# Optimization experiments

Measured on AMD Instinct MI355X. Metric: run time of the kernel, lower is better.

Reference implementation:

```python
import jax, jax.numpy as jnp
import numpy as np

B, C, T = 16, 128, 4096
Q, K = 8, 1024


def setup_inputs() -> dict:
    key = jax.random.key(0)
    k1, k2 = jax.random.split(key)
    latents = jax.random.normal(k1, (B, C, T), dtype=jnp.float32)
    embeddings = jax.random.normal(k2, (Q, K, C), dtype=jnp.float32)
    return {"latents": latents, "embeddings": embeddings}


def reference(latents, embeddings):
    # latents: [B, C, T]; embeddings: [Q, K, C]
    b, c, t = latents.shape
    q = embeddings.shape[0]
    flat = latents.transpose(0, 2, 1).reshape(-1, c)  # [N, C], N = B*T

    def stage(carry, emb):
        residual, qsum, closs = carry
        # squared euclidean distances [N, K] via expansion identity
        d = ((residual * residual).sum(axis=1, keepdims=True)
             - 2.0 * residual @ emb.T
             + (emb * emb).sum(axis=1))
        idx = jnp.argmin(d, axis=1)          # [N]
        quant = emb[idx]                     # [N, C] gather
        closs = closs + jnp.mean((residual - jax.lax.stop_gradient(quant)) ** 2)
        return (residual - quant, qsum + quant, closs), idx

    init = (flat, jnp.zeros_like(flat), jnp.zeros((), dtype=flat.dtype))
    (_, qsum, closs), codes = jax.lax.scan(stage, init, embeddings)

    quantized = qsum.reshape(b, t, c).transpose(0, 2, 1)       # [B, C, T]
    codes = codes.reshape(q, b, t).transpose(1, 0, 2)          # [B, Q, T]
    commitment_loss = closs / q
    codebook_loss = jnp.zeros((), dtype=latents.dtype)
    return quantized, codes, commitment_loss, codebook_loss
```

## Files before the change

### kernel.cpp

```cpp
#include <hip/hip_runtime.h>

#define Bq 16
#define Cc 128
#define Tt 4096
#define Qq 8
#define Kk 1024
#define Nn (Bq*Tt)

#define ROWS 128
#define NTC  256
#define KCH  32
#define NTILES (Kk/NTC)
#define KCHUNKS (Cc/KCH)
#define NCHUNK (NTILES*KCHUNKS)

typedef float f32x4 __attribute__((ext_vector_type(4)));
typedef float f32x8 __attribute__((ext_vector_type(8)));
typedef int   i32x8 __attribute__((ext_vector_type(8)));

static __device__ __forceinline__ f32x8 splat8(float x) {
    f32x8 v = {x, x, x, x, x, x, x, x};
    return v;
}

__global__ __launch_bounds__(256) void ee_kernel(const float* __restrict__ emb,
                                                 float* __restrict__ ee,
                                                 double* __restrict__ closs) {
    int i = blockIdx.x * 256 + threadIdx.x;
    if (i == 0) *closs = 0.0;
    if (i < Qq * Kk) {
        const float* e = emb + (size_t)i * Cc;
        float s0 = 0.f, s1 = 0.f, s2 = 0.f, s3 = 0.f;
#pragma unroll
        for (int c = 0; c < Cc; c += 4) {
            s0 = fmaf(e[c],     e[c],     s0);
            s1 = fmaf(e[c + 1], e[c + 1], s1);
            s2 = fmaf(e[c + 2], e[c + 2], s2);
            s3 = fmaf(e[c + 3], e[c + 3], s3);
        }
        ee[i] = (s0 + s1) + (s2 + s3);
    }
}

__global__ __launch_bounds__(512, 2) void vq_kernel(
    const float* __restrict__ latents,
    const float* __restrict__ emb,
    const float* __restrict__ ee,
    float* __restrict__ quantized,
    float* __restrict__ codes,
    double* __restrict__ closs)
{
    extern __shared__ float smem[];
    float* r_lds  = smem;
    float* B_lds  = smem + Cc * ROWS;
    float* rrp    = B_lds + 2 * KCH * NTC;
    float* rr_lds = rrp + 4 * ROWS;
    int*   win    = (int*)(rr_lds + ROWS);

    const int t   = threadIdx.x;
    const int tx  = t & 31;
    const int ty  = t >> 5;
    const int un  = t & 127;
    const int ukg = t >> 7;
    const int cl  = t >> 1;
    const int hk  = (t & 1) * 16;

    const int rowbase = blockIdx.x * ROWS;
    const int bb  = rowbase >> 12;
    const int tt0 = rowbase & (Tt - 1);

    {
        const float* lb = latents + (size_t)bb * Cc * Tt + tt0 + un;
        float part = 0.f;
#pragma unroll
        for (int j = 0; j < KCH; ++j) {
            int k = ukg * KCH + j;
            float v = lb[(size_t)k * Tt];
            r_lds[k * ROWS + un] = v;
            part = fmaf(v, v, part);
        }
        rrp[ukg * ROWS + un] = part;
    }
    __syncthreads();
    if (t < ROWS)
        rr_lds[t] = (rrp[t] + rrp[ROWS + t]) + (rrp[2 * ROWS + t] + rrp[3 * ROWS + t]);
    __syncthreads();

    for (int q = 0; q < Qq; ++q) {
        const float* eq = emb + (size_t)q * Kk * Cc;

        f32x8 best_ = splat8(3.4e38f);
        i32x8 bk_   = {0, 0, 0, 0, 0, 0, 0, 0};
        f32x8 rr8   = *(const f32x8*)&rr_lds[ty * 8];

        {
            const float* src = eq + (size_t)cl * Cc + hk;
            f32x4 pf0 = *(const f32x4*)(src);
            f32x4 pf1 = *(const f32x4*)(src + 4);
            f32x4 pf2 = *(const f32x4*)(src + 8);
            f32x4 pf3 = *(const f32x4*)(src + 12);
#pragma unroll
            for (int i2 = 0; i2 < 4; ++i2) B_lds[(hk +      i2) * NTC + cl] = pf0[i2];
#pragma unroll
            for (int i2 = 0; i2 < 4; ++i2) B_lds[(hk +  4 + i2) * NTC + cl] = pf1[i2];
#pragma unroll
            for (int i2 = 0; i2 < 4; ++i2) B_lds[(hk +  8 + i2) * NTC + cl] = pf2[i2];
#pragma unroll
            for (int i2 = 0; i2 < 4; ++i2) B_lds[(hk + 12 + i2) * NTC + cl] = pf3[i2];
        }
        __syncthreads();

        f32x8 acc0, acc1, acc2, acc3, acc4, acc5, acc6, acc7;

        for (int id = 0; id < NCHUNK; ++id) {
            const int nt  = id >> 2;
            const int kc  = id & 3;
            const int cur = id & 1;
            if (kc == 0) {
                acc0 = splat8(0.f); acc1 = splat8(0.f); acc2 = splat8(0.f); acc3 = splat8(0.f);
                acc4 = splat8(0.f); acc5 = splat8(0.f); acc6 = splat8(0.f); acc7 = splat8(0.f);
            }

            f32x4 pf0, pf1, pf2, pf3;
            if (id < NCHUNK - 1) {
                const int nid = id + 1;
                const float* src = eq + (size_t)(((nid >> 2) * NTC) + cl) * Cc
                                 + (nid & 3) * KCH + hk;
                pf0 = *(const f32x4*)(src);
                pf1 = *(const f32x4*)(src + 4);
                pf2 = *(const f32x4*)(src + 8);
                pf3 = *(const f32x4*)(src + 12);
            }

            const float* Bb = B_lds + cur * (KCH * NTC);
#pragma unroll 8
            for (int kk = 0; kk < KCH; ++kk) {
                f32x8 a_  = *(const f32x8*)&r_lds[(kc * KCH + kk) * ROWS + ty * 8];
                f32x4 blo = *(const f32x4*)&Bb[kk * NTC + tx * 4];
                f32x4 bhi = *(const f32x4*)&Bb[kk * NTC + 128 + tx * 4];
                f32x8 b_  = __builtin_shufflevector(blo, bhi, 0, 1, 2, 3, 4, 5, 6, 7);
                acc0 = __builtin_elementwise_fma(splat8(a_[0]), b_, acc0);
                acc1 = __builtin_elementwise_fma(splat8(a_[1]), b_, acc1);
                acc2 = __builtin_elementwise_fma(splat8(a_[2]), b_, acc2);
                acc3 = __builtin_elementwise_fma(splat8(a_[3]), b_, acc3);
                acc4 = __builtin_elementwise_fma(splat8(a_[4]), b_, acc4);
                acc5 = __builtin_elementwise_fma(splat8(a_[5]), b_, acc5);
                acc6 = __builtin_elementwise_fma(splat8(a_[6]), b_, acc6);
                acc7 = __builtin_elementwise_fma(splat8(a_[7]), b_, acc7);
            }

            if (id < NCHUNK - 1) {
                float* Bn = B_lds + (cur ^ 1) * (KCH * NTC);
#pragma unroll
                for (int i2 = 0; i2 < 4; ++i2) Bn[(hk +      i2) * NTC + cl] = pf0[i2];
#pragma unroll
                for (int i2 = 0; i2 < 4; ++i2) Bn[(hk +  4 + i2) * NTC + cl] = pf1[i2];
#pragma unroll
                for (int i2 = 0; i2 < 4; ++i2) Bn[(hk +  8 + i2) * NTC + cl] = pf2[i2];
#pragma unroll
                for (int i2 = 0; i2 < 4; ++i2) Bn[(hk + 12 + i2) * NTC + cl] = pf3[i2];
            }
            __syncthreads();

            if (kc == 3) {
                const int kb = nt * NTC + tx * 4;
                f32x4 eelo = *(const f32x4*)(ee + q * Kk + kb);
                f32x4 eehi = *(const f32x4*)(ee + q * Kk + kb + 128);
                f32x8 ee_  = __builtin_shufflevector(eelo, eehi, 0, 1, 2, 3, 4, 5, 6, 7);
#define FOLD_ROW(I_) {                                                        \
                f32x8 dv = __builtin_elementwise_fma(splat8(-2.0f), acc##I_,  \
                                                     splat8(rr8[I_])) + ee_;  \
                _Pragma("unroll")                                             \
                for (int c = 0; c < 8; ++c) {                                 \
                    float d = dv[c];                                          \
                    int code = kb + (c < 4 ? c : c + 124);                    \
                    bool lt = d < best_[I_];                                  \
                    best_[I_] = lt ? d : best_[I_];                           \
                    bk_[I_]   = lt ? code : bk_[I_];                          \
                } }
                FOLD_ROW(0) FOLD_ROW(1) FOLD_ROW(2) FOLD_ROW(3)
                FOLD_ROW(4) FOLD_ROW(5) FOLD_ROW(6) FOLD_ROW(7)
#undef FOLD_ROW
            }
        }

#pragma unroll
        for (int m = 1; m < 32; m <<= 1) {
#pragma unroll
            for (int i = 0; i < 8; ++i) {
                float od = __shfl_xor(best_[i], m);
                int   ok = __shfl_xor(bk_[i], m);
                bool rep = (od < best_[i]) || (od == best_[i] && ok < bk_[i]);
                best_[i] = rep ? od : best_[i];
                bk_[i]   = rep ? ok : bk_[i];
            }
        }
        if (tx == 0) {
#pragma unroll
            for (int i = 0; i < 8; ++i) {
                int row = ty * 8 + i;
                win[row] = bk_[i];
                codes[((size_t)bb * Qq + q) * Tt + tt0 + row] = (float)bk_[i];
            }
        }
        __syncthreads();

        {
            const float* er = eq + (size_t)win[un] * Cc + ukg * KCH;
            float part = 0.f;
#pragma unroll
            for (int j = 0; j < 8; ++j) {
                f32x4 ev = *(const f32x4*)(er + j * 4);
#pragma unroll
                for (int i2 = 0; i2 < 4; ++i2) {
                    int k = ukg * KCH + j * 4 + i2;
                    float rv = r_lds[k * ROWS + un] - ev[i2];
                    r_lds[k * ROWS + un] = rv;
                    part = fmaf(rv, rv, part);
                }
            }
            rrp[ukg * ROWS + un] = part;
        }
        __syncthreads();
        if (t < ROWS)
            rr_lds[t] = (rrp[t] + rrp[ROWS + t]) + (rrp[2 * ROWS + t] + rrp[3 * ROWS + t]);
        __syncthreads();
        if (t < 64) {
            double s = (double)rr_lds[t] + (double)rr_lds[t + 64];
#pragma unroll
            for (int off = 32; off; off >>= 1)
                s += __shfl_down(s, off);
            if (t == 0) atomicAdd(closs, s);
        }
    }

    {
        const float* lb = latents + (size_t)bb * Cc * Tt + tt0 + un;
        float* qb = quantized + (size_t)bb * Cc * Tt + tt0 + un;
#pragma unroll
        for (int j = 0; j < KCH; ++j) {
            int k = ukg * KCH + j;
            qb[(size_t)k * Tt] = lb[(size_t)k * Tt] - r_lds[k * ROWS + un];
        }
    }
}

__global__ void fin_kernel(const double* __restrict__ closs, float* __restrict__ loss_out) {
    loss_out[0] = (float)(*closs / (double)((size_t)Nn * Cc * Qq));
    loss_out[1] = 0.0f;
}

extern "C" void kernel_launch(void* const* d_in, const int* in_sizes, int n_in,
                              void* d_out, int out_size, void* d_ws, size_t ws_size,
                              hipStream_t stream) {
    const float* latents = (const float*)d_in[0];
    const float* emb     = (const float*)d_in[1];
    float* out       = (float*)d_out;
    float* quantized = out;
    float* codes     = out + (size_t)Bq * Cc * Tt;
    float* loss      = codes + (size_t)Bq * Qq * Tt;
    double* closs    = (double*)d_ws;
    float*  ee       = (float*)((char*)d_ws + 64);

    const size_t smem = (size_t)(Cc * ROWS + 2 * KCH * NTC + 4 * ROWS + ROWS) * sizeof(float)
                      + ROWS * sizeof(int);
    (void)hipFuncSetAttribute((const void*)vq_kernel,
                              hipFuncAttributeMaxDynamicSharedMemorySize, (int)smem);

    ee_kernel<<<(Qq * Kk + 255) / 256, 256, 0, stream>>>(emb, ee, closs);
    vq_kernel<<<Nn / ROWS, 512, smem, stream>>>(latents, emb, ee, quantized, codes, closs);
    fin_kernel<<<1, 1, 0, stream>>>(closs, loss);
}
```

Before: 1.759 ms.

## Widen codebook tile to 512 columns with 1024-thread single-buffered blocks

Doubles the block to 1024 threads and the codebook tile to 512 columns. Each thread row group now spans a full 64-lane wavefront, and the per-thread accumulators are split into low and high 4-wide halves. The double-buffered B tile in LDS becomes a single buffer guarded by two barriers per chunk, which keeps LDS use roughly flat while halving the number of tile passes. The trade-offs are lost load/compute overlap, extra barriers, and a launch bound of (1024,4) that may force heavy register limits and spills.

```diff
diff --git a/kernel.cpp b/kernel.cpp
--- a/kernel.cpp
+++ b/kernel.cpp
@@ -8,7 +8,7 @@
 #define Nn (Bq*Tt)
 
 #define ROWS 128
-#define NTC  256
+#define NTC  512
 #define KCH  32
 #define NTILES (Kk/NTC)
 #define KCHUNKS (Cc/KCH)
@@ -18,7 +18,11 @@
 typedef float f32x8 __attribute__((ext_vector_type(8)));
 typedef int   i32x8 __attribute__((ext_vector_type(8)));
 
-static __device__ __forceinline__ f32x8 splat8(float x) {
+static __device__ __forceinline__ f32x4 splat4(float x) {
+    f32x4 v = {x, x, x, x};
+    return v;
+}
+static __device__ __forceinline__ f32x8 splat8f(float x) {
     f32x8 v = {x, x, x, x, x, x, x, x};
     return v;
 }
@@ -42,7 +46,7 @@
     }
 }
 
-__global__ __launch_bounds__(512, 2) void vq_kernel(
+__global__ __launch_bounds__(1024, 4) void vq_kernel(
     const float* __restrict__ latents,
     const float* __restrict__ emb,
     const float* __restrict__ ee,
@@ -53,13 +57,13 @@
     extern __shared__ float smem[];
     float* r_lds  = smem;
     float* B_lds  = smem + Cc * ROWS;
-    float* rrp    = B_lds + 2 * KCH * NTC;
-    float* rr_lds = rrp + 4 * ROWS;
+    float* rrp    = B_lds + KCH * NTC;
+    float* rr_lds = rrp + 8 * ROWS;
     int*   win    = (int*)(rr_lds + ROWS);
 
     const int t   = threadIdx.x;
-    const int tx  = t & 31;
-    const int ty  = t >> 5;
+    const int tx  = t & 63;
+    const int ty  = t >> 6;
     const int un  = t & 127;
     const int ukg = t >> 7;
     const int cl  = t >> 1;
@@ -73,8 +77,8 @@
         const float* lb = latents + (size_t)bb * Cc * Tt + tt0 + un;
         float part = 0.f;
 #pragma unroll
-        for (int j = 0; j < KCH; ++j) {
-            int k = ukg * KCH + j;
+        for (int j = 0; j < 16; ++j) {
+            int k = ukg * 16 + j;
             float v = lb[(size_t)k * Tt];
             r_lds[k * ROWS + un] = v;
             part = fmaf(v, v, part);
@@ -83,13 +87,14 @@
     }
     __syncthreads();
     if (t < ROWS)
-        rr_lds[t] = (rrp[t] + rrp[ROWS + t]) + (rrp[2 * ROWS + t] + rrp[3 * ROWS + t]);
+        rr_lds[t] = ((rrp[t] + rrp[ROWS + t]) + (rrp[2*ROWS + t] + rrp[3*ROWS + t]))
+                  + ((rrp[4*ROWS + t] + rrp[5*ROWS + t]) + (rrp[6*ROWS + t] + rrp[7*ROWS + t]));
     __syncthreads();
 
     for (int q = 0; q < Qq; ++q) {
         const float* eq = emb + (size_t)q * Kk * Cc;
 
-        f32x8 best_ = splat8(3.4e38f);
+        f32x8 best_ = splat8f(3.4e38f);
         i32x8 bk_   = {0, 0, 0, 0, 0, 0, 0, 0};
         f32x8 rr8   = *(const f32x8*)&rr_lds[ty * 8];
 
@@ -110,15 +115,17 @@
         }
         __syncthreads();
 
-        f32x8 acc0, acc1, acc2, acc3, acc4, acc5, acc6, acc7;
+        f32x4 aL0, aL1, aL2, aL3, aL4, aL5, aL6, aL7;
+        f32x4 aH0, aH1, aH2, aH3, aH4, aH5, aH6, aH7;
 
         for (int id = 0; id < NCHUNK; ++id) {
-            const int nt  = id >> 2;
-            const int kc  = id & 3;
-            const int cur = id & 1;
+            const int nt = id >> 2;
+            const int kc = id & 3;
             if (kc == 0) {
-                acc0 = splat8(0.f); acc1 = splat8(0.f); acc2 = splat8(0.f); acc3 = splat8(0.f);
-                acc4 = splat8(0.f); acc5 = splat8(0.f); acc6 = splat8(0.f); acc7 = splat8(0.f);
+                aL0 = splat4(0.f); aL1 = splat4(0.f); aL2 = splat4(0.f); aL3 = splat4(0.f);
+                aL4 = splat4(0.f); aL5 = splat4(0.f); aL6 = splat4(0.f); aL7 = splat4(0.f);
+                aH0 = splat4(0.f); aH1 = splat4(0.f); aH2 = splat4(0.f); aH3 = splat4(0.f);
+                aH4 = splat4(0.f); aH5 = splat4(0.f); aH6 = splat4(0.f); aH7 = splat4(0.f);
             }
 
             f32x4 pf0, pf1, pf2, pf3;
@@ -132,51 +139,64 @@
                 pf3 = *(const f32x4*)(src + 12);
             }
 
-            const float* Bb = B_lds + cur * (KCH * NTC);
 #pragma unroll 8
             for (int kk = 0; kk < KCH; ++kk) {
                 f32x8 a_  = *(const f32x8*)&r_lds[(kc * KCH + kk) * ROWS + ty * 8];
-                f32x4 blo = *(const f32x4*)&Bb[kk * NTC + tx * 4];
-                f32x4 bhi = *(const f32x4*)&Bb[kk * NTC + 128 + tx * 4];
-                f32x8 b_  = __builtin_shufflevector(blo, bhi, 0, 1, 2, 3, 4, 5, 6, 7);
-                acc0 = __builtin_elementwise_fma(splat8(a_[0]), b_, acc0);
-                acc1 = __builtin_elementwise_fma(splat8(a_[1]), b_, acc1);
-                acc2 = __builtin_elementwise_fma(splat8(a_[2]), b_, acc2);
-                acc3 = __builtin_elementwise_fma(splat8(a_[3]), b_, acc3);
-                acc4 = __builtin_elementwise_fma(splat8(a_[4]), b_, acc4);
-                acc5 = __builtin_elementwise_fma(splat8(a_[5]), b_, acc5);
-                acc6 = __builtin_elementwise_fma(splat8(a_[6]), b_, acc6);
-                acc7 = __builtin_elementwise_fma(splat8(a_[7]), b_, acc7);
+                f32x4 blo = *(const f32x4*)&B_lds[kk * NTC + tx * 4];
+                f32x4 bhi = *(const f32x4*)&B_lds[kk * NTC + 256 + tx * 4];
+                aL0 = __builtin_elementwise_fma(splat4(a_[0]), blo, aL0);
+                aH0 = __builtin_elementwise_fma(splat4(a_[0]), bhi, aH0);
+                aL1 = __builtin_elementwise_fma(splat4(a_[1]), blo, aL1);
+                aH1 = __builtin_elementwise_fma(splat4(a_[1]), bhi, aH1);
+                aL2 = __builtin_elementwise_fma(splat4(a_[2]), blo, aL2);
+                aH2 = __builtin_elementwise_fma(splat4(a_[2]), bhi, aH2);
+                aL3 = __builtin_elementwise_fma(splat4(a_[3]), blo, aL3);
+                aH3 = __builtin_elementwise_fma(splat4(a_[3]), bhi, aH3);
+                aL4 = __builtin_elementwise_fma(splat4(a_[4]), blo, aL4);
+                aH4 = __builtin_elementwise_fma(splat4(a_[4]), bhi, aH4);
+                aL5 = __builtin_elementwise_fma(splat4(a_[5]), blo, aL5);
+                aH5 = __builtin_elementwise_fma(splat4(a_[5]), bhi, aH5);
+                aL6 = __builtin_elementwise_fma(splat4(a_[6]), blo, aL6);
+                aH6 = __builtin_elementwise_fma(splat4(a_[6]), bhi, aH6);
+                aL7 = __builtin_elementwise_fma(splat4(a_[7]), blo, aL7);
+                aH7 = __builtin_elementwise_fma(splat4(a_[7]), bhi, aH7);
             }
 
             if (id < NCHUNK - 1) {
-                float* Bn = B_lds + (cur ^ 1) * (KCH * NTC);
-#pragma unroll
-                for (int i2 = 0; i2 < 4; ++i2) Bn[(hk +      i2) * NTC + cl] = pf0[i2];
-#pragma unroll
-                for (int i2 = 0; i2 < 4; ++i2) Bn[(hk +  4 + i2) * NTC + cl] = pf1[i2];
-#pragma unroll
-                for (int i2 = 0; i2 < 4; ++i2) Bn[(hk +  8 + i2) * NTC + cl] = pf2[i2];
-#pragma unroll
-                for (int i2 = 0; i2 < 4; ++i2) Bn[(hk + 12 + i2) * NTC + cl] = pf3[i2];
-            }
-            __syncthreads();
+                __syncthreads();
+#pragma unroll
+                for (int i2 = 0; i2 < 4; ++i2) B_lds[(hk +      i2) * NTC + cl] = pf0[i2];
+#pragma unroll
+                for (int i2 = 0; i2 < 4; ++i2) B_lds[(hk +  4 + i2) * NTC + cl] = pf1[i2];
+#pragma unroll
+                for (int i2 = 0; i2 < 4; ++i2) B_lds[(hk +  8 + i2) * NTC + cl] = pf2[i2];
+#pragma unroll
+                for (int i2 = 0; i2 < 4; ++i2) B_lds[(hk + 12 + i2) * NTC + cl] = pf3[i2];
+                __syncthreads();
+            }
 
             if (kc == 3) {
                 const int kb = nt * NTC + tx * 4;
                 f32x4 eelo = *(const f32x4*)(ee + q * Kk + kb);
-                f32x4 eehi = *(const f32x4*)(ee + q * Kk + kb + 128);
-                f32x8 ee_  = __builtin_shufflevector(eelo, eehi, 0, 1, 2, 3, 4, 5, 6, 7);
+                f32x4 eehi = *(const f32x4*)(ee + q * Kk + kb + 256);
 #define FOLD_ROW(I_) {                                                        \
-                f32x8 dv = __builtin_elementwise_fma(splat8(-2.0f), acc##I_,  \
-                                                     splat8(rr8[I_])) + ee_;  \
+                f32x4 dl = __builtin_elementwise_fma(splat4(-2.0f), aL##I_,   \
+                                                     splat4(rr8[I_])) + eelo; \
                 _Pragma("unroll")                                             \
-                for (int c = 0; c < 8; ++c) {                                 \
-                    float d = dv[c];                                          \
-                    int code = kb + (c < 4 ? c : c + 124);                    \
+                for (int c = 0; c < 4; ++c) {                                 \
+                    float d = dl[c];                                          \
                     bool lt = d < best_[I_];                                  \
                     best_[I_] = lt ? d : best_[I_];                           \
-                    bk_[I_]   = lt ? code : bk_[I_];                          \
+                    bk_[I_]   = lt ? (kb + c) : bk_[I_];                      \
+                }                                                             \
+                f32x4 dh = __builtin_elementwise_fma(splat4(-2.0f), aH##I_,   \
+                                                     splat4(rr8[I_])) + eehi; \
+                _Pragma("unroll")                                             \
+                for (int c = 0; c < 4; ++c) {                                 \
+                    float d = dh[c];                                          \
+                    bool lt = d < best_[I_];                                  \
+                    best_[I_] = lt ? d : best_[I_];                           \
+                    bk_[I_]   = lt ? (kb + 256 + c) : bk_[I_];                \
                 } }
                 FOLD_ROW(0) FOLD_ROW(1) FOLD_ROW(2) FOLD_ROW(3)
                 FOLD_ROW(4) FOLD_ROW(5) FOLD_ROW(6) FOLD_ROW(7)
@@ -185,7 +205,7 @@
         }
 
 #pragma unroll
-        for (int m = 1; m < 32; m <<= 1) {
+        for (int m = 1; m < 64; m <<= 1) {
 #pragma unroll
             for (int i = 0; i < 8; ++i) {
                 float od = __shfl_xor(best_[i], m);
@@ -206,14 +226,14 @@
         __syncthreads();
 
         {
-            const float* er = eq + (size_t)win[un] * Cc + ukg * KCH;
+            const float* er = eq + (size_t)win[un] * Cc + ukg * 16;
             float part = 0.f;
 #pragma unroll
-            for (int j = 0; j < 8; ++j) {
+            for (int j = 0; j < 4; ++j) {
                 f32x4 ev = *(const f32x4*)(er + j * 4);
 #pragma unroll
                 for (int i2 = 0; i2 < 4; ++i2) {
-                    int k = ukg * KCH + j * 4 + i2;
+                    int k = ukg * 16 + j * 4 + i2;
                     float rv = r_lds[k * ROWS + un] - ev[i2];
                     r_lds[k * ROWS + un] = rv;
                     part = fmaf(rv, rv, part);
@@ -223,7 +243,8 @@
         }
         __syncthreads();
         if (t < ROWS)
-            rr_lds[t] = (rrp[t] + rrp[ROWS + t]) + (rrp[2 * ROWS + t] + rrp[3 * ROWS + t]);
+            rr_lds[t] = ((rrp[t] + rrp[ROWS + t]) + (rrp[2*ROWS + t] + rrp[3*ROWS + t]))
+                      + ((rrp[4*ROWS + t] + rrp[5*ROWS + t]) + (rrp[6*ROWS + t] + rrp[7*ROWS + t]));
         __syncthreads();
         if (t < 64) {
             double s = (double)rr_lds[t] + (double)rr_lds[t + 64];
@@ -238,8 +259,8 @@
         const float* lb = latents + (size_t)bb * Cc * Tt + tt0 + un;
         float* qb = quantized + (size_t)bb * Cc * Tt + tt0 + un;
 #pragma unroll
-        for (int j = 0; j < KCH; ++j) {
-            int k = ukg * KCH + j;
+        for (int j = 0; j < 16; ++j) {
+            int k = ukg * 16 + j;
             qb[(size_t)k * Tt] = lb[(size_t)k * Tt] - r_lds[k * ROWS + un];
         }
     }
@@ -262,12 +283,12 @@
     double* closs    = (double*)d_ws;
     float*  ee       = (float*)((char*)d_ws + 64);
 
-    const size_t smem = (size_t)(Cc * ROWS + 2 * KCH * NTC + 4 * ROWS + ROWS) * sizeof(float)
+    const size_t smem = (size_t)(Cc * ROWS + KCH * NTC + 8 * ROWS + ROWS) * sizeof(float)
                       + ROWS * sizeof(int);
     (void)hipFuncSetAttribute((const void*)vq_kernel,
                               hipFuncAttributeMaxDynamicSharedMemorySize, (int)smem);
 
     ee_kernel<<<(Qq * Kk + 255) / 256, 256, 0, stream>>>(emb, ee, closs);
-    vq_kernel<<<Nn / ROWS, 512, smem, stream>>>(latents, emb, ee, quantized, codes, closs);
+    vq_kernel<<<Nn / ROWS, 1024, smem, stream>>>(latents, emb, ee, quantized, codes, closs);
     fin_kernel<<<1, 1, 0, stream>>>(closs, loss);
 }
```

Measured after the change: 2.340 ms. 33.0% more time.
